# Kernel optimization log

Hardware: AMD Instinct MI355X
Metric: run time of the kernel (lower is better)

## Reference

```python
import jax, jax.numpy as jnp
import numpy as np

N, DEG, F = 500000, 16, 128
H1, H2, OUT = 256, 256, 128


def setup_inputs() -> dict:
    key = jax.random.key(0)
    ks = jax.random.split(key, 8)
    s = lambda fan_in: 1.0 / np.sqrt(fan_in)
    return {
        "message": jax.random.normal(ks[0], (N, DEG, F), dtype=jnp.float32),
        "features": jax.random.normal(ks[1], (N, F), dtype=jnp.float32),
        "global_features": jax.random.normal(ks[2], (N, F), dtype=jnp.float32),
        "W1": jax.random.normal(ks[3], (3 * F, H1), dtype=jnp.float32) * s(3 * F),
        "b1": jnp.zeros((H1,), dtype=jnp.float32),
        "W2": jax.random.normal(ks[4], (H1, H2), dtype=jnp.float32) * s(H1),
        "b2": jnp.zeros((H2,), dtype=jnp.float32),
        "W3": jax.random.normal(ks[5], (H2, OUT), dtype=jnp.float32) * s(H2),
        "b3": jnp.zeros((OUT,), dtype=jnp.float32),
    }


def reference(message, features, global_features, W1, b1, W2, b2, W3, b3):
    # mailbox sum-aggregate over neighbors: [N, deg, F] -> [N, F]
    agg = jnp.sum(message, axis=1)
    # concat aggregated messages with node + global features: [N, 3F]
    x = jnp.concatenate([agg, features, global_features], axis=1)
    # MLP: Linear+ReLU, Linear+ReLU, Linear
    h = jax.nn.relu(x @ W1 + b1)
    h = jax.nn.relu(h @ W2 + b2)
    out = h @ W3 + b3
    # row-wise L2 (Frobenius over dim=1) normalization
    norm = jnp.linalg.norm(out, axis=1, keepdims=True)
    return out / (norm + 1e-8)
```

## Files before the change

kernel.cpp:

```cpp
#include <hip/hip_runtime.h>


typedef short short8   __attribute__((ext_vector_type(8)));
typedef short short4_t __attribute__((ext_vector_type(4)));
typedef float f32x4    __attribute__((ext_vector_type(4)));

#define SWZ(row, off) ((off) ^ (((row) & 7) << 4))

__device__ __forceinline__ unsigned short f2bf(float f) {
    unsigned int u = __float_as_uint(f);
    u += 0x7fffu + ((u >> 16) & 1u);
    return (unsigned short)(u >> 16);
}

__global__ void prep_weights(const float* __restrict__ W1,
                             const float* __restrict__ W2,
                             const float* __restrict__ W3,
                             short* __restrict__ pw1,
                             short* __restrict__ pw2,
                             short* __restrict__ pw3) {
    int idx = blockIdx.x * 256 + threadIdx.x;
    if (idx < 98304) {
        int j = idx & 7, l = (idx >> 3) & 63, g = idx >> 9;
        int ks = g % 12, tn = g / 12;
        int n = tn * 16 + (l & 15);
        int k = ks * 32 + ((l >> 4) << 3) + j;
        pw1[idx] = (short)f2bf(W1[k * 256 + n]);
    } else if (idx < 98304 + 65536) {
        int e = idx - 98304;
        int j = e & 7, l = (e >> 3) & 63, g = e >> 9;
        int ks = g & 7, tn = g >> 3;
        int n = tn * 16 + (l & 15);
        int k = ks * 32 + ((l >> 4) << 3) + j;
        pw2[e] = (short)f2bf(W2[k * 256 + n]);
    } else if (idx < 98304 + 65536 + 32768) {
        int e = idx - 98304 - 65536;
        int j = e & 7, l = (e >> 3) & 63, g = e >> 9;
        int ks = g & 7, tn = g >> 3;
        int n = tn * 16 + (l & 15);
        int k = ks * 32 + ((l >> 4) << 3) + j;
        pw3[e] = (short)f2bf(W3[k * 128 + n]);
    }
}

__global__ __launch_bounds__(256) void agg_kernel(
    const float* __restrict__ msg, short* __restrict__ agg, int n_rows)
{
    const int w = threadIdx.x >> 6;
    const int l = threadIdx.x & 63;
    const long long pb = (long long)blockIdx.x * 8 + 2 * w;
    if (pb >= n_rows) return;

    const f32x4* base = (const f32x4*)((const char*)msg + pb * 8192);
    f32x4 tA[8], tB[8];
    const bool okB = (pb + 1) < n_rows;
    #pragma unroll
    for (int i = 0; i < 8; ++i) tA[i] = __builtin_nontemporal_load(base + i * 64 + l);
    if (okB) {
        #pragma unroll
        for (int i = 0; i < 8; ++i) tB[i] = __builtin_nontemporal_load(base + (8 + i) * 64 + l);
    } else {
        #pragma unroll
        for (int i = 0; i < 8; ++i) tB[i] = (f32x4){0.f, 0.f, 0.f, 0.f};
    }
    f32x4 sA = ((tA[0] + tA[1]) + (tA[2] + tA[3])) + ((tA[4] + tA[5]) + (tA[6] + tA[7]));
    f32x4 sB = ((tB[0] + tB[1]) + (tB[2] + tB[3])) + ((tB[4] + tB[5]) + (tB[6] + tB[7]));
    #pragma unroll
    for (int c = 0; c < 4; ++c) {
        sA[c] += __shfl_xor(sA[c], 32);
        sB[c] += __shfl_xor(sB[c], 32);
    }
    f32x4 s = (l < 32) ? sA : sB;
    short4_t s4;
    s4[0] = (short)f2bf(s[0]); s4[1] = (short)f2bf(s[1]);
    s4[2] = (short)f2bf(s[2]); s4[3] = (short)f2bf(s[3]);
    const long long orow = pb + (l >> 5);
    if (orow < n_rows)
        *(short4_t*)(agg + orow * 128 + (l & 31) * 4) = s4;
}

__global__ __launch_bounds__(256, 4) void node_net(
    const short* __restrict__ aggb,
    const float* __restrict__ feat,
    const float* __restrict__ glob,
    const float* __restrict__ b1v,
    const float* __restrict__ b2v,
    const float* __restrict__ b3v,
    const short* __restrict__ pw1,
    const short* __restrict__ pw2,
    const short* __restrict__ pw3,
    float* __restrict__ out,
    int n_rows)
{
    __shared__ char lds[32768];
    char* regA = lds;
    char* regB = lds + 16384;

    const int tid  = threadIdx.x;
    const int lane = tid & 63;
    const int w    = tid >> 6;
    const int lr   = lane & 15;
    const int lk   = lane >> 4;
    const long long r0 = (long long)blockIdx.x * 32;

    const f32x4 zero4 = {0.f, 0.f, 0.f, 0.f};

    f32x4 fr[4], gr[4];
    #pragma unroll
    for (int q = 0; q < 4; ++q) {
        int r = (tid >> 5) + q * 8;
        long long row = r0 + r;
        fr[q] = zero4; gr[q] = zero4;
        if (row < n_rows) {
            fr[q] = ((const f32x4*)feat)[row * 32 + (tid & 31)];
            gr[q] = ((const f32x4*)glob)[row * 32 + (tid & 31)];
        }
    }

    #pragma unroll
    for (int pass = 0; pass < 2; ++pass) {
        int r = tid >> 3;
        int c = (tid & 7) + 8 * pass;
        long long row = r0 + r;
        short8 v = {0, 0, 0, 0, 0, 0, 0, 0};
        if (row < n_rows) v = *(const short8*)(aggb + row * 128 + c * 8);
        *(short8*)(regB + SWZ(r, r * 256 + c * 16)) = v;
    }
    __syncthreads();

    #pragma unroll
    for (int q = 0; q < 4; ++q) {
        int r = (tid >> 5) + q * 8;
        short4_t s4;
        s4[0] = (short)f2bf(fr[q][0]); s4[1] = (short)f2bf(fr[q][1]);
        s4[2] = (short)f2bf(fr[q][2]); s4[3] = (short)f2bf(fr[q][3]);
        *(short4_t*)(regA + SWZ(r, r * 256 + (tid & 31) * 8)) = s4;
    }

    f32x4 acc1[2][4];
    #pragma unroll
    for (int ri = 0; ri < 2; ++ri)
        #pragma unroll
        for (int ci = 0; ci < 4; ++ci) acc1[ri][ci] = zero4;

    #pragma unroll
    for (int s = 0; s < 4; ++s) {
        short8 a[2], b[4];
        #pragma unroll
        for (int ri = 0; ri < 2; ++ri) {
            int row = ri * 16 + lr;
            a[ri] = *(const short8*)(regB + SWZ(row, row * 256 + s * 64 + lk * 16));
        }
        #pragma unroll
        for (int ci = 0; ci < 4; ++ci) {
            int tn = w * 4 + ci;
            b[ci] = *(const short8*)(pw1 + (((tn * 12 + s) * 64 + lane) << 3));
        }
        #pragma unroll
        for (int ri = 0; ri < 2; ++ri)
            #pragma unroll
            for (int ci = 0; ci < 4; ++ci)
                acc1[ri][ci] = __builtin_amdgcn_mfma_f32_16x16x32_bf16(
                    a[ri], b[ci], acc1[ri][ci], 0, 0, 0);
    }
    __syncthreads();

    #pragma unroll
    for (int q = 0; q < 4; ++q) {
        int r = (tid >> 5) + q * 8;
        short4_t s4;
        s4[0] = (short)f2bf(gr[q][0]); s4[1] = (short)f2bf(gr[q][1]);
        s4[2] = (short)f2bf(gr[q][2]); s4[3] = (short)f2bf(gr[q][3]);
        *(short4_t*)(regB + 8192 + SWZ(r, r * 256 + (tid & 31) * 8)) = s4;
    }

    #pragma unroll
    for (int s = 0; s < 4; ++s) {
        short8 a[2], b[4];
        #pragma unroll
        for (int ri = 0; ri < 2; ++ri) {
            int row = ri * 16 + lr;
            a[ri] = *(const short8*)(regA + SWZ(row, row * 256 + s * 64 + lk * 16));
        }
        #pragma unroll
        for (int ci = 0; ci < 4; ++ci) {
            int tn = w * 4 + ci;
            b[ci] = *(const short8*)(pw1 + (((tn * 12 + 4 + s) * 64 + lane) << 3));
        }
        #pragma unroll
        for (int ri = 0; ri < 2; ++ri)
            #pragma unroll
            for (int ci = 0; ci < 4; ++ci)
                acc1[ri][ci] = __builtin_amdgcn_mfma_f32_16x16x32_bf16(
                    a[ri], b[ci], acc1[ri][ci], 0, 0, 0);
    }
    __syncthreads();

    #pragma unroll
    for (int s = 0; s < 4; ++s) {
        short8 a[2], b[4];
        #pragma unroll
        for (int ri = 0; ri < 2; ++ri) {
            int row = ri * 16 + lr;
            a[ri] = *(const short8*)(regB + 8192 + SWZ(row, row * 256 + s * 64 + lk * 16));
        }
        #pragma unroll
        for (int ci = 0; ci < 4; ++ci) {
            int tn = w * 4 + ci;
            b[ci] = *(const short8*)(pw1 + (((tn * 12 + 8 + s) * 64 + lane) << 3));
        }
        #pragma unroll
        for (int ri = 0; ri < 2; ++ri)
            #pragma unroll
            for (int ci = 0; ci < 4; ++ci)
                acc1[ri][ci] = __builtin_amdgcn_mfma_f32_16x16x32_bf16(
                    a[ri], b[ci], acc1[ri][ci], 0, 0, 0);
    }

    #pragma unroll
    for (int ci = 0; ci < 4; ++ci) {
        int col = w * 64 + ci * 16 + lr;
        float bias = b1v[col];
        #pragma unroll
        for (int ri = 0; ri < 2; ++ri)
            #pragma unroll
            for (int i = 0; i < 4; ++i) {
                int row = ri * 16 + lk * 4 + i;
                float v = fmaxf(acc1[ri][ci][i] + bias, 0.f);
                *(short*)(regA + SWZ(row, row * 512 + col * 2)) = (short)f2bf(v);
            }
    }
    __syncthreads();

    f32x4 acc2[2][4];
    #pragma unroll
    for (int ri = 0; ri < 2; ++ri)
        #pragma unroll
        for (int ci = 0; ci < 4; ++ci) acc2[ri][ci] = zero4;

    #pragma unroll
    for (int s = 0; s < 8; ++s) {
        short8 a[2], b[4];
        #pragma unroll
        for (int ri = 0; ri < 2; ++ri) {
            int row = ri * 16 + lr;
            a[ri] = *(const short8*)(regA + SWZ(row, row * 512 + s * 64 + lk * 16));
        }
        #pragma unroll
        for (int ci = 0; ci < 4; ++ci) {
            int tn = w * 4 + ci;
            b[ci] = *(const short8*)(pw2 + (((tn * 8 + s) * 64 + lane) << 3));
        }
        #pragma unroll
        for (int ri = 0; ri < 2; ++ri)
            #pragma unroll
            for (int ci = 0; ci < 4; ++ci)
                acc2[ri][ci] = __builtin_amdgcn_mfma_f32_16x16x32_bf16(
                    a[ri], b[ci], acc2[ri][ci], 0, 0, 0);
    }

    #pragma unroll
    for (int ci = 0; ci < 4; ++ci) {
        int col = w * 64 + ci * 16 + lr;
        float bias = b2v[col];
        #pragma unroll
        for (int ri = 0; ri < 2; ++ri)
            #pragma unroll
            for (int i = 0; i < 4; ++i) {
                int row = ri * 16 + lk * 4 + i;
                float v = fmaxf(acc2[ri][ci][i] + bias, 0.f);
                *(short*)(regB + SWZ(row, row * 512 + col * 2)) = (short)f2bf(v);
            }
    }
    __syncthreads();

    f32x4 acc3[2][2];
    #pragma unroll
    for (int ri = 0; ri < 2; ++ri)
        #pragma unroll
        for (int ci = 0; ci < 2; ++ci) acc3[ri][ci] = zero4;

    #pragma unroll
    for (int s = 0; s < 8; ++s) {
        short8 a[2], b[2];
        #pragma unroll
        for (int ri = 0; ri < 2; ++ri) {
            int row = ri * 16 + lr;
            a[ri] = *(const short8*)(regB + SWZ(row, row * 512 + s * 64 + lk * 16));
        }
        #pragma unroll
        for (int ci = 0; ci < 2; ++ci) {
            int tn = w * 2 + ci;
            b[ci] = *(const short8*)(pw3 + (((tn * 8 + s) * 64 + lane) << 3));
        }
        #pragma unroll
        for (int ri = 0; ri < 2; ++ri)
            #pragma unroll
            for (int ci = 0; ci < 2; ++ci)
                acc3[ri][ci] = __builtin_amdgcn_mfma_f32_16x16x32_bf16(
                    a[ri], b[ci], acc3[ri][ci], 0, 0, 0);
    }

    #pragma unroll
    for (int ci = 0; ci < 2; ++ci) {
        int col = w * 32 + ci * 16 + lr;
        float bias = b3v[col];
        #pragma unroll
        for (int ri = 0; ri < 2; ++ri)
            #pragma unroll
            for (int i = 0; i < 4; ++i) {
                int row = ri * 16 + lk * 4 + i;
                float v = acc3[ri][ci][i] + bias;
                *(float*)(regA + SWZ(row, row * 512 + col * 4)) = v;
            }
    }
    __syncthreads();

    #pragma unroll
    for (int pass = 0; pass < 4; ++pass) {
        const int r  = (tid >> 5) + pass * 8;
        const int fl = tid & 31;
        f32x4 v = *(const f32x4*)(regA + SWZ(r, r * 512 + fl * 16));
        float ss = v[0]*v[0] + v[1]*v[1] + v[2]*v[2] + v[3]*v[3];
        ss += __shfl_xor(ss, 1, 32);
        ss += __shfl_xor(ss, 2, 32);
        ss += __shfl_xor(ss, 4, 32);
        ss += __shfl_xor(ss, 8, 32);
        ss += __shfl_xor(ss, 16, 32);
        float inv = 1.f / (sqrtf(ss) + 1e-8f);
        long long row = r0 + r;
        if (row < n_rows) {
            f32x4 o = v * inv;
            ((f32x4*)out)[row * 32 + fl] = o;
        }
    }
}

extern "C" void kernel_launch(void* const* d_in, const int* in_sizes, int n_in,
                              void* d_out, int out_size, void* d_ws, size_t ws_size,
                              hipStream_t stream) {
    const float* msg  = (const float*)d_in[0];
    const float* feat = (const float*)d_in[1];
    const float* glob = (const float*)d_in[2];
    const float* W1   = (const float*)d_in[3];
    const float* b1   = (const float*)d_in[4];
    const float* W2   = (const float*)d_in[5];
    const float* b2   = (const float*)d_in[6];
    const float* W3   = (const float*)d_in[7];
    const float* b3   = (const float*)d_in[8];
    float* out = (float*)d_out;

    const int n_rows = in_sizes[1] / 128;

    short* pw1  = (short*)d_ws;
    short* pw2  = pw1 + 98304;
    short* pw3  = pw2 + 65536;
    short* aggb = pw3 + 32768;

    hipLaunchKernelGGL(prep_weights, dim3(768), dim3(256), 0, stream,
                       W1, W2, W3, pw1, pw2, pw3);

    const int ablocks = (n_rows + 7) / 8;
    hipLaunchKernelGGL(agg_kernel, dim3(ablocks), dim3(256), 0, stream,
                       msg, aggb, n_rows);

    const int nblocks = (n_rows + 31) / 32;
    hipLaunchKernelGGL(node_net, dim3(nblocks), dim3(256), 0, stream,
                       aggb, feat, glob, b1, b2, b3, pw1, pw2, pw3, out, n_rows);
}
```

Before: 1.276 ms.

## Software-pipeline weight fragment loads through a 3-deep register ring across layers

Weight B-fragments now go through a 3-stage register ring that is prefetched across K-steps and across layer boundaries, so layer-2 and layer-3 weights load while the previous layer's MFMAs run. All three layer-1 input slabs (agg, features, global) are staged into LDS together, which removes two barriers, and the biases are hoisted into registers at kernel start. LDS grows from 32KB to 40KB and the ring needs 12 extra short8 registers, which may lower occupancy under the 4-blocks launch bound.

```diff
diff --git a/kernel.cpp b/kernel.cpp
--- a/kernel.cpp
+++ b/kernel.cpp
@@ -92,9 +92,8 @@
     float* __restrict__ out,
     int n_rows)
 {
-    __shared__ char lds[32768];
-    char* regA = lds;
-    char* regB = lds + 16384;
+    __shared__ char lds[40960];
+    char* ldsH = lds + 24576;
 
     const int tid  = threadIdx.x;
     const int lane = tid & 63;
@@ -104,6 +103,22 @@
     const long long r0 = (long long)blockIdx.x * 32;
 
     const f32x4 zero4 = {0.f, 0.f, 0.f, 0.f};
+
+    short8 ring[3][4];
+    #pragma unroll
+    for (int k0 = 0; k0 < 3; ++k0)
+        #pragma unroll
+        for (int ci = 0; ci < 4; ++ci)
+            ring[k0][ci] = *(const short8*)(pw1 + ((((w * 4 + ci) * 12 + k0) * 64 + lane) << 3));
+
+    float bias1[4], bias2[4], bias3[2];
+    #pragma unroll
+    for (int ci = 0; ci < 4; ++ci) {
+        bias1[ci] = b1v[w * 64 + ci * 16 + lr];
+        bias2[ci] = b2v[w * 64 + ci * 16 + lr];
+    }
+    #pragma unroll
+    for (int ci = 0; ci < 2; ++ci) bias3[ci] = b3v[w * 32 + ci * 16 + lr];
 
     f32x4 fr[4], gr[4];
     #pragma unroll
@@ -116,26 +131,34 @@
             gr[q] = ((const f32x4*)glob)[row * 32 + (tid & 31)];
         }
     }
+    short8 av[2];
+    #pragma unroll
+    for (int pass = 0; pass < 2; ++pass) {
+        int r = tid >> 3;
+        long long row = r0 + r;
+        av[pass] = (short8){0, 0, 0, 0, 0, 0, 0, 0};
+        if (row < n_rows)
+            av[pass] = *(const short8*)(aggb + row * 128 + ((tid & 7) + 8 * pass) * 8);
+    }
 
     #pragma unroll
     for (int pass = 0; pass < 2; ++pass) {
         int r = tid >> 3;
         int c = (tid & 7) + 8 * pass;
-        long long row = r0 + r;
-        short8 v = {0, 0, 0, 0, 0, 0, 0, 0};
-        if (row < n_rows) v = *(const short8*)(aggb + row * 128 + c * 8);
-        *(short8*)(regB + SWZ(r, r * 256 + c * 16)) = v;
-    }
-    __syncthreads();
-
+        *(short8*)(lds + SWZ(r, r * 256 + c * 16)) = av[pass];
+    }
     #pragma unroll
     for (int q = 0; q < 4; ++q) {
         int r = (tid >> 5) + q * 8;
-        short4_t s4;
-        s4[0] = (short)f2bf(fr[q][0]); s4[1] = (short)f2bf(fr[q][1]);
-        s4[2] = (short)f2bf(fr[q][2]); s4[3] = (short)f2bf(fr[q][3]);
-        *(short4_t*)(regA + SWZ(r, r * 256 + (tid & 31) * 8)) = s4;
-    }
+        short4_t sf, sg;
+        sf[0] = (short)f2bf(fr[q][0]); sf[1] = (short)f2bf(fr[q][1]);
+        sf[2] = (short)f2bf(fr[q][2]); sf[3] = (short)f2bf(fr[q][3]);
+        sg[0] = (short)f2bf(gr[q][0]); sg[1] = (short)f2bf(gr[q][1]);
+        sg[2] = (short)f2bf(gr[q][2]); sg[3] = (short)f2bf(gr[q][3]);
+        *(short4_t*)(lds + 8192  + SWZ(r, r * 256 + (tid & 31) * 8)) = sf;
+        *(short4_t*)(lds + 16384 + SWZ(r, r * 256 + (tid & 31) * 8)) = sg;
+    }
+    __syncthreads();
 
     f32x4 acc1[2][4];
     #pragma unroll
@@ -144,174 +167,127 @@
         for (int ci = 0; ci < 4; ++ci) acc1[ri][ci] = zero4;
 
     #pragma unroll
-    for (int s = 0; s < 4; ++s) {
-        short8 a[2], b[4];
+    for (int ks = 0; ks < 12; ++ks) {
+        const int s = ks & 3, p = ks >> 2;
+        short8 a[2];
         #pragma unroll
         for (int ri = 0; ri < 2; ++ri) {
             int row = ri * 16 + lr;
-            a[ri] = *(const short8*)(regB + SWZ(row, row * 256 + s * 64 + lk * 16));
-        }
-        #pragma unroll
-        for (int ci = 0; ci < 4; ++ci) {
-            int tn = w * 4 + ci;
-            b[ci] = *(const short8*)(pw1 + (((tn * 12 + s) * 64 + lane) << 3));
+            a[ri] = *(const short8*)(lds + p * 8192 + SWZ(row, row * 256 + s * 64 + lk * 16));
         }
         #pragma unroll
         for (int ri = 0; ri < 2; ++ri)
             #pragma unroll
             for (int ci = 0; ci < 4; ++ci)
                 acc1[ri][ci] = __builtin_amdgcn_mfma_f32_16x16x32_bf16(
-                    a[ri], b[ci], acc1[ri][ci], 0, 0, 0);
+                    a[ri], ring[ks % 3][ci], acc1[ri][ci], 0, 0, 0);
+        if (ks < 9) {
+            #pragma unroll
+            for (int ci = 0; ci < 4; ++ci)
+                ring[ks % 3][ci] = *(const short8*)(pw1 + ((((w * 4 + ci) * 12 + (ks + 3)) * 64 + lane) << 3));
+        } else {
+            #pragma unroll
+            for (int ci = 0; ci < 4; ++ci)
+                ring[ks % 3][ci] = *(const short8*)(pw2 + ((((w * 4 + ci) * 8 + (ks - 9)) * 64 + lane) << 3));
+        }
+    }
+
+    #pragma unroll
+    for (int ci = 0; ci < 4; ++ci) {
+        int col = w * 64 + ci * 16 + lr;
+        #pragma unroll
+        for (int ri = 0; ri < 2; ++ri)
+            #pragma unroll
+            for (int i = 0; i < 4; ++i) {
+                int row = ri * 16 + lk * 4 + i;
+                float v = fmaxf(acc1[ri][ci][i] + bias1[ci], 0.f);
+                *(short*)(ldsH + SWZ(row, row * 512 + col * 2)) = (short)f2bf(v);
+            }
     }
     __syncthreads();
 
-    #pragma unroll
-    for (int q = 0; q < 4; ++q) {
-        int r = (tid >> 5) + q * 8;
-        short4_t s4;
-        s4[0] = (short)f2bf(gr[q][0]); s4[1] = (short)f2bf(gr[q][1]);
-        s4[2] = (short)f2bf(gr[q][2]); s4[3] = (short)f2bf(gr[q][3]);
-        *(short4_t*)(regB + 8192 + SWZ(r, r * 256 + (tid & 31) * 8)) = s4;
-    }
-
-    #pragma unroll
-    for (int s = 0; s < 4; ++s) {
-        short8 a[2], b[4];
+    f32x4 acc2[2][4];
+    #pragma unroll
+    for (int ri = 0; ri < 2; ++ri)
+        #pragma unroll
+        for (int ci = 0; ci < 4; ++ci) acc2[ri][ci] = zero4;
+
+    #pragma unroll
+    for (int ks = 0; ks < 8; ++ks) {
+        short8 a[2];
         #pragma unroll
         for (int ri = 0; ri < 2; ++ri) {
             int row = ri * 16 + lr;
-            a[ri] = *(const short8*)(regA + SWZ(row, row * 256 + s * 64 + lk * 16));
-        }
-        #pragma unroll
-        for (int ci = 0; ci < 4; ++ci) {
-            int tn = w * 4 + ci;
-            b[ci] = *(const short8*)(pw1 + (((tn * 12 + 4 + s) * 64 + lane) << 3));
-        }
-        #pragma unroll
-        for (int ri = 0; ri < 2; ++ri)
-            #pragma unroll
-            for (int ci = 0; ci < 4; ++ci)
-                acc1[ri][ci] = __builtin_amdgcn_mfma_f32_16x16x32_bf16(
-                    a[ri], b[ci], acc1[ri][ci], 0, 0, 0);
+            a[ri] = *(const short8*)(ldsH + SWZ(row, row * 512 + ks * 64 + lk * 16));
+        }
+        #pragma unroll
+        for (int ri = 0; ri < 2; ++ri)
+            #pragma unroll
+            for (int ci = 0; ci < 4; ++ci)
+                acc2[ri][ci] = __builtin_amdgcn_mfma_f32_16x16x32_bf16(
+                    a[ri], ring[ks % 3][ci], acc2[ri][ci], 0, 0, 0);
+        if (ks < 5) {
+            #pragma unroll
+            for (int ci = 0; ci < 4; ++ci)
+                ring[ks % 3][ci] = *(const short8*)(pw2 + ((((w * 4 + ci) * 8 + (ks + 3)) * 64 + lane) << 3));
+        } else {
+            #pragma unroll
+            for (int ci = 0; ci < 2; ++ci)
+                ring[ks % 3][ci] = *(const short8*)(pw3 + ((((w * 2 + ci) * 8 + (ks - 5)) * 64 + lane) << 3));
+        }
+    }
+
+    #pragma unroll
+    for (int ci = 0; ci < 4; ++ci) {
+        int col = w * 64 + ci * 16 + lr;
+        #pragma unroll
+        for (int ri = 0; ri < 2; ++ri)
+            #pragma unroll
+            for (int i = 0; i < 4; ++i) {
+                int row = ri * 16 + lk * 4 + i;
+                float v = fmaxf(acc2[ri][ci][i] + bias2[ci], 0.f);
+                *(short*)(lds + SWZ(row, row * 512 + col * 2)) = (short)f2bf(v);
+            }
     }
     __syncthreads();
 
-    #pragma unroll
-    for (int s = 0; s < 4; ++s) {
-        short8 a[2], b[4];
+    f32x4 acc3[2][2];
+    #pragma unroll
+    for (int ri = 0; ri < 2; ++ri)
+        #pragma unroll
+        for (int ci = 0; ci < 2; ++ci) acc3[ri][ci] = zero4;
+
+    #pragma unroll
+    for (int ks = 0; ks < 8; ++ks) {
+        short8 a[2];
         #pragma unroll
         for (int ri = 0; ri < 2; ++ri) {
             int row = ri * 16 + lr;
-            a[ri] = *(const short8*)(regB + 8192 + SWZ(row, row * 256 + s * 64 + lk * 16));
-        }
-        #pragma unroll
-        for (int ci = 0; ci < 4; ++ci) {
-            int tn = w * 4 + ci;
-            b[ci] = *(const short8*)(pw1 + (((tn * 12 + 8 + s) * 64 + lane) << 3));
-        }
-        #pragma unroll
-        for (int ri = 0; ri < 2; ++ri)
-            #pragma unroll
-            for (int ci = 0; ci < 4; ++ci)
-                acc1[ri][ci] = __builtin_amdgcn_mfma_f32_16x16x32_bf16(
-                    a[ri], b[ci], acc1[ri][ci], 0, 0, 0);
-    }
-
-    #pragma unroll
-    for (int ci = 0; ci < 4; ++ci) {
-        int col = w * 64 + ci * 16 + lr;
-        float bias = b1v[col];
+            a[ri] = *(const short8*)(lds + SWZ(row, row * 512 + ks * 64 + lk * 16));
+        }
+        #pragma unroll
+        for (int ri = 0; ri < 2; ++ri)
+            #pragma unroll
+            for (int ci = 0; ci < 2; ++ci)
+                acc3[ri][ci] = __builtin_amdgcn_mfma_f32_16x16x32_bf16(
+                    a[ri], ring[(ks + 2) % 3][ci], acc3[ri][ci], 0, 0, 0);
+        if (ks < 5) {
+            #pragma unroll
+            for (int ci = 0; ci < 2; ++ci)
+                ring[(ks + 2) % 3][ci] = *(const short8*)(pw3 + ((((w * 2 + ci) * 8 + (ks + 3)) * 64 + lane) << 3));
+        }
+    }
+
+    #pragma unroll
+    for (int ci = 0; ci < 2; ++ci) {
+        int col = w * 32 + ci * 16 + lr;
         #pragma unroll
         for (int ri = 0; ri < 2; ++ri)
             #pragma unroll
             for (int i = 0; i < 4; ++i) {
                 int row = ri * 16 + lk * 4 + i;
-                float v = fmaxf(acc1[ri][ci][i] + bias, 0.f);
-                *(short*)(regA + SWZ(row, row * 512 + col * 2)) = (short)f2bf(v);
-            }
-    }
-    __syncthreads();
-
-    f32x4 acc2[2][4];
-    #pragma unroll
-    for (int ri = 0; ri < 2; ++ri)
-        #pragma unroll
-        for (int ci = 0; ci < 4; ++ci) acc2[ri][ci] = zero4;
-
-    #pragma unroll
-    for (int s = 0; s < 8; ++s) {
-        short8 a[2], b[4];
-        #pragma unroll
-        for (int ri = 0; ri < 2; ++ri) {
-            int row = ri * 16 + lr;
-            a[ri] = *(const short8*)(regA + SWZ(row, row * 512 + s * 64 + lk * 16));
-        }
-        #pragma unroll
-        for (int ci = 0; ci < 4; ++ci) {
-            int tn = w * 4 + ci;
-            b[ci] = *(const short8*)(pw2 + (((tn * 8 + s) * 64 + lane) << 3));
-        }
-        #pragma unroll
-        for (int ri = 0; ri < 2; ++ri)
-            #pragma unroll
-            for (int ci = 0; ci < 4; ++ci)
-                acc2[ri][ci] = __builtin_amdgcn_mfma_f32_16x16x32_bf16(
-                    a[ri], b[ci], acc2[ri][ci], 0, 0, 0);
-    }
-
-    #pragma unroll
-    for (int ci = 0; ci < 4; ++ci) {
-        int col = w * 64 + ci * 16 + lr;
-        float bias = b2v[col];
-        #pragma unroll
-        for (int ri = 0; ri < 2; ++ri)
-            #pragma unroll
-            for (int i = 0; i < 4; ++i) {
-                int row = ri * 16 + lk * 4 + i;
-                float v = fmaxf(acc2[ri][ci][i] + bias, 0.f);
-                *(short*)(regB + SWZ(row, row * 512 + col * 2)) = (short)f2bf(v);
-            }
-    }
-    __syncthreads();
-
-    f32x4 acc3[2][2];
-    #pragma unroll
-    for (int ri = 0; ri < 2; ++ri)
-        #pragma unroll
-        for (int ci = 0; ci < 2; ++ci) acc3[ri][ci] = zero4;
-
-    #pragma unroll
-    for (int s = 0; s < 8; ++s) {
-        short8 a[2], b[2];
-        #pragma unroll
-        for (int ri = 0; ri < 2; ++ri) {
-            int row = ri * 16 + lr;
-            a[ri] = *(const short8*)(regB + SWZ(row, row * 512 + s * 64 + lk * 16));
-        }
-        #pragma unroll
-        for (int ci = 0; ci < 2; ++ci) {
-            int tn = w * 2 + ci;
-            b[ci] = *(const short8*)(pw3 + (((tn * 8 + s) * 64 + lane) << 3));
-        }
-        #pragma unroll
-        for (int ri = 0; ri < 2; ++ri)
-            #pragma unroll
-            for (int ci = 0; ci < 2; ++ci)
-                acc3[ri][ci] = __builtin_amdgcn_mfma_f32_16x16x32_bf16(
-                    a[ri], b[ci], acc3[ri][ci], 0, 0, 0);
-    }
-
-    #pragma unroll
-    for (int ci = 0; ci < 2; ++ci) {
-        int col = w * 32 + ci * 16 + lr;
-        float bias = b3v[col];
-        #pragma unroll
-        for (int ri = 0; ri < 2; ++ri)
-            #pragma unroll
-            for (int i = 0; i < 4; ++i) {
-                int row = ri * 16 + lk * 4 + i;
-                float v = acc3[ri][ci][i] + bias;
-                *(float*)(regA + SWZ(row, row * 512 + col * 4)) = v;
+                float v = acc3[ri][ci][i] + bias3[ci];
+                *(float*)(ldsH + SWZ(row, row * 512 + col * 4)) = v;
             }
     }
     __syncthreads();
@@ -320,7 +296,7 @@
     for (int pass = 0; pass < 4; ++pass) {
         const int r  = (tid >> 5) + pass * 8;
         const int fl = tid & 31;
-        f32x4 v = *(const f32x4*)(regA + SWZ(r, r * 512 + fl * 16));
+        f32x4 v = *(const f32x4*)(ldsH + SWZ(r, r * 512 + fl * 16));
         float ss = v[0]*v[0] + v[1]*v[1] + v[2]*v[2] + v[3]*v[3];
         ss += __shfl_xor(ss, 1, 32);
         ss += __shfl_xor(ss, 2, 32);
```

Result: slower. 1.328 ms (+4.1%).
